# Performance work log

Measured on AMD Instinct MI355X. Metric: run time of the kernel, lower is better.

## Reference

```python
import jax, jax.numpy as jnp
import numpy as np

S, B, I, H, O = 512, 64, 128, 512, 1


def setup_inputs() -> dict:
    key = jax.random.key(0)
    ks = jax.random.split(key, 12)
    s = 1.0 / np.sqrt(H)
    u = lambda k, shape: jax.random.uniform(k, shape, jnp.float32, -s, s)
    return {
        "inputs": jax.random.normal(ks[0], (S, B, I), jnp.float32),
        # pre nn.RNN (1 layer, tanh)
        "W_ih_pre": u(ks[1], (H, I)),
        "W_hh_pre": u(ks[2], (H, H)),
        "b_ih_pre": u(ks[3], (H,)),
        "b_hh_pre": u(ks[4], (H,)),
        # post nn.RNNCell (input_size=hidden_size)
        "W_ih_post": u(ks[5], (H, H)),
        "W_hh_post": u(ks[6], (H, H)),
        "b_ih_post": u(ks[7], (H,)),
        "b_hh_post": u(ks[8], (H,)),
        # fc head
        "W_fc": u(ks[9], (O, H)),
        "b_fc": u(ks[10], (O,)),
    }


def reference(inputs, W_ih_pre, W_hh_pre, b_ih_pre, b_hh_pre,
              W_ih_post, W_hh_post, b_ih_post, b_hh_post, W_fc, b_fc):
    batch = inputs.shape[1]
    hidden = W_ih_pre.shape[0]
    h0 = jnp.zeros((batch, hidden), inputs.dtype)

    # ---- pre RNN over time (tanh cell), inputs are (S, B, I) ----
    x_proj = jnp.einsum('sbi,hi->sbh', inputs, W_ih_pre) + b_ih_pre

    def pre_step(h, x_t):
        h = jnp.tanh(x_t + h @ W_hh_pre.T + b_hh_pre)
        return h, h

    _, out_pre = jax.lax.scan(pre_step, h0, x_proj)  # (S, B, H)

    # ---- attention loop: exactly `hidden` sequential steps ----
    def attn_step(h, _):
        # dot-prod alignment: sum over feature dim -> (S, B)
        scores = jnp.einsum('sbh,bh->sb', out_pre, h)
        w = jax.nn.softmax(scores, axis=0)          # softmax over seq dim
        ctx = jnp.einsum('sbh,sb->bh', out_pre, w)  # weighted sum -> (B, H)
        h = jnp.tanh(ctx @ W_ih_post.T + b_ih_post + h @ W_hh_post.T + b_hh_post)
        return h, None

    h_post, _ = jax.lax.scan(attn_step, h0, None, length=hidden)
    return h_post @ W_fc.T + b_fc  # (B, O)
```

## Files before the change

### kernel.cpp

```cpp
#include <hip/hip_runtime.h>
#include <math.h>

#define NWG 256
#define NTHR 512
static constexpr int S = 512, B = 64, I = 128, H = 512;

static constexpr size_t OFF_BUF0   = 0;
static constexpr size_t OFF_PCTX   = (size_t)S * B * H;
static constexpr size_t OFF_H3X    = OFF_PCTX + (size_t)64 * 4 * 520;
static constexpr size_t OFF_ACTR   = OFF_H3X + (size_t)64 * 4 * 128;
static constexpr size_t OFF_HCTR   = OFF_ACTR + (size_t)64 * 4 * 16;
static constexpr size_t OFF_GFLAGS = OFF_HCTR + (size_t)64 * 4 * 16;
static constexpr size_t OFF_END    = OFF_GFLAGS + (size_t)256 * 16;

typedef float f32x2 __attribute__((ext_vector_type(2)));
typedef float f32x4 __attribute__((ext_vector_type(4)));

__device__ __forceinline__ void st_g1(float* p, float v) {
  asm volatile("global_store_dword %0, %1, off sc0 sc1" :: "v"(p), "v"(v) : "memory");
}
__device__ __forceinline__ void st_g2(float* p, f32x2 v) {
  asm volatile("global_store_dwordx2 %0, %1, off sc0 sc1" :: "v"(p), "v"(v) : "memory");
}
__device__ __forceinline__ void st_gu(unsigned* p, unsigned v) {
  asm volatile("global_store_dword %0, %1, off sc0 sc1" :: "v"(p), "v"(v) : "memory");
}
__device__ __forceinline__ f32x4 ld_g4(const float* p) {
  f32x4 v;
  asm volatile("global_load_dwordx4 %0, %1, off sc0 sc1\n\ts_waitcnt vmcnt(0)"
               : "=&v"(v) : "v"(p) : "memory");
  return v;
}
__device__ __forceinline__ void ld_3c(const float* v0, const float* v1, const float* v2,
                                      const float* m0, const float* m1, const float* m2,
                                      float& a, float& b, float& c,
                                      f32x2& x, f32x2& y, f32x2& z) {
  asm volatile("global_load_dword %0, %6, off sc0 sc1\n\t"
               "global_load_dword %1, %7, off sc0 sc1\n\t"
               "global_load_dword %2, %8, off sc0 sc1\n\t"
               "global_load_dwordx2 %3, %9, off sc0 sc1\n\t"
               "global_load_dwordx2 %4, %10, off sc0 sc1\n\t"
               "global_load_dwordx2 %5, %11, off sc0 sc1\n\t"
               "s_waitcnt vmcnt(0)"
               : "=&v"(a), "=&v"(b), "=&v"(c), "=&v"(x), "=&v"(y), "=&v"(z)
               : "v"(v0), "v"(v1), "v"(v2), "v"(m0), "v"(m1), "v"(m2) : "memory");
}
__device__ __forceinline__ void poll3_ge(const unsigned* p0, const unsigned* p1,
                                         const unsigned* p2, unsigned tgt) {
  unsigned a, b, c;
  do {
    asm volatile("global_load_dword %0, %3, off sc0 sc1\n\t"
                 "global_load_dword %1, %4, off sc0 sc1\n\t"
                 "global_load_dword %2, %5, off sc0 sc1\n\t"
                 "s_waitcnt vmcnt(0)"
                 : "=&v"(a), "=&v"(b), "=&v"(c)
                 : "v"(p0), "v"(p1), "v"(p2) : "memory");
  } while (a < tgt || b < tgt || c < tgt);
}
__device__ __forceinline__ void vm_drain() { asm volatile("s_waitcnt vmcnt(0)" ::: "memory"); }

__device__ __forceinline__ void gbar_all(unsigned* gflags, int wg, unsigned gen) {
  __syncthreads();
  if (threadIdx.x == 0)
    __hip_atomic_store(gflags + (size_t)wg * 16, gen, __ATOMIC_RELEASE, __HIP_MEMORY_SCOPE_AGENT);
  if (threadIdx.x < 256) {
    while (__hip_atomic_load(gflags + (size_t)threadIdx.x * 16, __ATOMIC_ACQUIRE,
                             __HIP_MEMORY_SCOPE_AGENT) < gen) {}
  }
  __syncthreads();
}

__global__ __launch_bounds__(NTHR, 2) void attn_fused(
    const float* __restrict__ inputs,
    const float* __restrict__ Wih_pre, const float* __restrict__ Whh_pre,
    const float* __restrict__ bih_pre, const float* __restrict__ bhh_pre,
    const float* __restrict__ Wih_post, const float* __restrict__ Whh_post,
    const float* __restrict__ bih_post, const float* __restrict__ bhh_post,
    const float* __restrict__ Wfc, const float* __restrict__ bfc,
    float* __restrict__ out, float* __restrict__ ws)
{
  float* buf0  = ws + OFF_BUF0;
  float* pctxg = ws + OFF_PCTX;
  float* h3xg  = ws + OFF_H3X;
  unsigned* actrg  = (unsigned*)(ws + OFF_ACTR);
  unsigned* hctrg  = (unsigned*)(ws + OFF_HCTR);
  unsigned* gflags = (unsigned*)(ws + OFF_GFLAGS);

  const int wg   = blockIdx.x;
  const int tid  = threadIdx.x;
  const int lane = tid & 63;
  const int wv   = tid >> 6;
  const int b    = wg & 63;
  const int part = wg >> 6;
  const int q1 = (part + 1) & 3, q2 = (part + 2) & 3, q3 = (part + 3) & 3;

  unsigned* hc_own = hctrg + ((size_t)b * 4 + part) * 16;
  unsigned* hc1 = hctrg + ((size_t)b * 4 + q1) * 16;
  unsigned* hc2 = hctrg + ((size_t)b * 4 + q2) * 16;
  unsigned* hc3 = hctrg + ((size_t)b * 4 + q3) * 16;
  unsigned* ac_own = actrg + ((size_t)b * 4 + part) * 16;
  unsigned* ac1 = actrg + ((size_t)b * 4 + q1) * 16;
  unsigned* ac2 = actrg + ((size_t)b * 4 + q2) * 16;
  unsigned* ac3 = actrg + ((size_t)b * 4 + q3) * 16;

  __shared__ float smem[8208];

  {
    const int h = tid;
    float4 Wr[32];
    const float4* wrow = (const float4*)(Wih_pre + (size_t)h * I);
    #pragma unroll
    for (int c = 0; c < 32; ++c) Wr[c] = wrow[c];
    const float bias = bih_pre[h] + bhh_pre[h];
    const int r0 = wg * 128;
    for (int t2 = 0; t2 < 2; ++t2) {
      __syncthreads();
      const float4* src = (const float4*)(inputs + (size_t)(r0 + t2 * 64) * I);
      for (int idx = tid; idx < 64 * I / 4; idx += NTHR)
        ((float4*)smem)[idx] = src[idx];
      __syncthreads();
      for (int r = 0; r < 64; ++r) {
        const float4* arow = (const float4*)(smem + r * I);
        float acc0 = 0.f, acc1 = 0.f;
        #pragma unroll
        for (int c = 0; c < 32; c += 2) {
          float4 a0 = arow[c], a1 = arow[c + 1];
          acc0 += a0.x * Wr[c].x + a0.y * Wr[c].y + a0.z * Wr[c].z + a0.w * Wr[c].w;
          acc1 += a1.x * Wr[c+1].x + a1.y * Wr[c+1].y + a1.z * Wr[c+1].z + a1.w * Wr[c+1].w;
        }
        buf0[(size_t)(r0 + t2 * 64 + r) * H + h] = acc0 + acc1 + bias;
      }
    }
  }
  gbar_all(gflags, wg, 1u);

  const int j  = part * 128 + (tid >> 2);
  const int kq = tid & 3;
  {
    float4 wpre[32];
    const float4* wrow = (const float4*)(Whh_pre + (size_t)j * H);
    #pragma unroll
    for (int i = 0; i < 32; ++i) wpre[i] = wrow[4 * i + kq];

    smem[tid] = 0.f;
    __syncthreads();

    for (int t = 0; t < S; ++t) {
      float* brow = buf0 + ((size_t)t * B + b) * H;
      float xp = brow[j];
      const float4* hst4 = (const float4*)smem;
      float d = 0.f;
      #pragma unroll
      for (int i = 0; i < 32; ++i) {
        float4 hv = hst4[4 * i + kq];
        d += wpre[i].x * hv.x + wpre[i].y * hv.y + wpre[i].z * hv.z + wpre[i].w * hv.w;
      }
      d += __shfl_xor(d, 1);
      d += __shfl_xor(d, 2);
      float hnew = tanhf(xp + d);
      const int par = (t + 1) & 1;
      float* slot = pctxg + (((size_t)b * 2 + par) * 4 + part) * 128;
      if (kq == 0) {
        brow[j] = hnew;
        st_g1(slot + (tid >> 2), hnew);
      }
      vm_drain();
      __syncthreads();
      if (tid == 0) st_gu(hc_own, (unsigned)(t + 1));
      poll3_ge(hc1, hc2, hc3, (unsigned)(t + 1));
      if (tid < 128) {
        f32x4 hv = ld_g4(pctxg + (((size_t)b * 2 + par) * 4) * 128 + (size_t)tid * 4);
        ((float4*)smem)[tid] = float4{hv.x, hv.y, hv.z, hv.w};
      }
      __syncthreads();
    }
  }
  gbar_all(gflags, wg, 2u);

  float4 ga[16], gb[16];
  {
    const int s0 = part * 128 + wv * 16;
    #pragma unroll
    for (int i = 0; i < 16; ++i) {
      const float* row = buf0 + ((size_t)(s0 + i) * B + b) * H;
      ga[i] = *(const float4*)(row + lane * 4);
      gb[i] = *(const float4*)(row + 256 + lane * 4);
    }
  }

  float4 wih[32], whh[32];
  {
    const float4* wr1 = (const float4*)(Wih_post + (size_t)j * H);
    const float4* wr2 = (const float4*)(Whh_post + (size_t)j * H);
    #pragma unroll
    for (int i = 0; i < 32; ++i) { wih[i] = wr1[4 * i + kq]; whh[i] = wr2[4 * i + kq]; }
  }
  const float bp3 = bih_post[j] + bhh_post[j];

  float* blk_own = pctxg + ((size_t)b * 4 + part) * 520;
  float* blk1 = pctxg + ((size_t)b * 4 + q1) * 520;
  float* blk2 = pctxg + ((size_t)b * 4 + q2) * 520;
  float* blk3 = pctxg + ((size_t)b * 4 + q3) * 520;

  smem[tid] = 0.f;
  __syncthreads();

  for (int u = 0; u < H; ++u) {
    float mstar, lsum;
    {
      float4 h0v = ((const float4*)smem)[lane];
      float4 h1v = ((const float4*)smem)[64 + lane];
      float p[16];
      #pragma unroll
      for (int i = 0; i < 16; ++i)
        p[i] = ga[i].x * h0v.x + ga[i].y * h0v.y + ga[i].z * h0v.z + ga[i].w * h0v.w
             + gb[i].x * h1v.x + gb[i].y * h1v.y + gb[i].z * h1v.z + gb[i].w * h1v.w;
      #pragma unroll
      for (int off = 32; off > 0; off >>= 1) {
        #pragma unroll
        for (int i = 0; i < 16; ++i) p[i] += __shfl_xor(p[i], off);
      }
      float m = p[0];
      #pragma unroll
      for (int i = 1; i < 16; ++i) m = fmaxf(m, p[i]);
      float l = 0.f;
      float4 c0{0.f,0.f,0.f,0.f}, c1{0.f,0.f,0.f,0.f};
      #pragma unroll
      for (int i = 0; i < 16; ++i) {
        float e = __expf(p[i] - m);
        l += e;
        c0.x += e * ga[i].x;  c0.y += e * ga[i].y;  c0.z += e * ga[i].z;  c0.w += e * ga[i].w;
        c1.x += e * gb[i].x;  c1.y += e * gb[i].y;  c1.z += e * gb[i].z;  c1.w += e * gb[i].w;
      }
      float* ctx_lds = smem + 1024;
      float* ml_lds  = smem + 5120;
      *(float4*)(ctx_lds + wv * 512 + lane * 4)       = c0;
      *(float4*)(ctx_lds + wv * 512 + 256 + lane * 4) = c1;
      if (lane == 0) { ml_lds[wv * 2] = m; ml_lds[wv * 2 + 1] = l; }
      __syncthreads();
      mstar = ml_lds[0];
      #pragma unroll
      for (int w = 1; w < 8; ++w) mstar = fmaxf(mstar, ml_lds[w * 2]);
      lsum = 0.f;
      float csum = 0.f;
      #pragma unroll
      for (int w = 0; w < 8; ++w) {
        float sc = __expf(ml_lds[w * 2] - mstar);
        lsum += sc * ml_lds[w * 2 + 1];
        csum += sc * ctx_lds[w * 512 + tid];
      }
      smem[512 + tid] = csum;
      st_g1(blk_own + tid, csum);
      if (tid == 0) st_g2(blk_own + 512, f32x2{mstar, lsum});
      vm_drain();
      __syncthreads();
      if (tid == 0) st_gu(ac_own, (unsigned)(u + 1));
    }

    {
      poll3_ge(ac1, ac2, ac3, (unsigned)(u + 1));
      float v1, v2, v3; f32x2 mlA, mlB, mlC;
      ld_3c(blk1 + tid, blk2 + tid, blk3 + tid,
            blk1 + 512, blk2 + 512, blk3 + 512, v1, v2, v3, mlA, mlB, mlC);
      float mb = fmaxf(fmaxf(mstar, mlA.x), fmaxf(mlB.x, mlC.x));
      float s0 = __expf(mstar - mb), s1 = __expf(mlA.x - mb);
      float s2 = __expf(mlB.x - mb), s3 = __expf(mlC.x - mb);
      float inv = 1.0f / (s0 * lsum + s1 * mlA.y + s2 * mlB.y + s3 * mlC.y);
      float cval = (s0 * smem[512 + tid] + s1 * v1 + s2 * v2 + s3 * v3) * inv;
      smem[1024 + tid] = cval;
      __syncthreads();
      const float4* ctx4 = (const float4*)(smem + 1024);
      const float4* hh4  = (const float4*)smem;
      float acc = 0.f;
      #pragma unroll
      for (int i = 0; i < 32; ++i) {
        float4 cv = ctx4[4 * i + kq];
        float4 hv = hh4[4 * i + kq];
        acc += wih[i].x * cv.x + wih[i].y * cv.y + wih[i].z * cv.z + wih[i].w * cv.w
             + whh[i].x * hv.x + whh[i].y * hv.y + whh[i].z * hv.z + whh[i].w * hv.w;
      }
      acc += __shfl_xor(acc, 1);
      acc += __shfl_xor(acc, 2);
      float hnew = tanhf(acc + bp3);
      if (kq == 0) st_g1(h3xg + ((size_t)b * 4 + part) * 128 + (tid >> 2), hnew);
      vm_drain();
      __syncthreads();
      if (tid == 0) st_gu(hc_own, (unsigned)(513 + u));
      poll3_ge(hc1, hc2, hc3, (unsigned)(513 + u));
      if (tid < 128) {
        f32x4 hv = ld_g4(h3xg + (size_t)b * 4 * 128 + (size_t)tid * 4);
        ((float4*)smem)[tid] = float4{hv.x, hv.y, hv.z, hv.w};
      }
      __syncthreads();
    }
  }

  if (part == 0) {
    float pv = smem[tid] * Wfc[tid];
    #pragma unroll
    for (int off = 32; off > 0; off >>= 1) pv += __shfl_xor(pv, off);
    __syncthreads();
    if (lane == 0) smem[5120 + wv] = pv;
    __syncthreads();
    if (tid == 0) {
      float s = 0.f;
      #pragma unroll
      for (int w = 0; w < 8; ++w) s += smem[5120 + w];
      out[b] = s + bfc[0];
    }
  }
}

extern "C" void kernel_launch(void* const* d_in, const int* in_sizes, int n_in,
                              void* d_out, int out_size, void* d_ws, size_t ws_size,
                              hipStream_t stream) {
  (void)in_sizes; (void)n_in; (void)out_size; (void)ws_size;
  const float* inputs   = (const float*)d_in[0];
  const float* Wih_pre  = (const float*)d_in[1];
  const float* Whh_pre  = (const float*)d_in[2];
  const float* bih_pre  = (const float*)d_in[3];
  const float* bhh_pre  = (const float*)d_in[4];
  const float* Wih_post = (const float*)d_in[5];
  const float* Whh_post = (const float*)d_in[6];
  const float* bih_post = (const float*)d_in[7];
  const float* bhh_post = (const float*)d_in[8];
  const float* Wfc      = (const float*)d_in[9];
  const float* bfc      = (const float*)d_in[10];
  float* out = (float*)d_out;
  float* ws  = (float*)d_ws;

  hipMemsetAsync((char*)d_ws + OFF_ACTR * sizeof(float), 0,
                 (OFF_END - OFF_ACTR) * sizeof(float), stream);

  attn_fused<<<dim3(NWG), dim3(NTHR), 0, stream>>>(
      inputs, Wih_pre, Whh_pre, bih_pre, bhh_pre,
      Wih_post, Whh_post, bih_post, bhh_post, Wfc, bfc, out, ws);
}
```

Before: 14.23 ms.

## Stop attention loop at exact fixed point and rebalance post-cell weight storage

After each attention step, every block checks whether the new hidden state is bitwise identical to the previous one and leaves the loop if so. The step depends only on h, so the remaining iterations would repeat the same state and the result stays exact. The post-cell weights are also split so that most of W_ih stays in registers, its tail sits in LDS, and W_hh is streamed from global memory. The W_hh product is computed early, before the cross-block wait. Only one wave polls the cross-block counters, and launch bounds drop to one block per CU. The gain depends on how quickly the inputs converge, and the extra check and barriers add cost to every step.

After: 19.90 ms. 39.8% more time.

```diff
diff --git a/kernel.cpp b/kernel.cpp
--- a/kernel.cpp
+++ b/kernel.cpp
@@ -8,13 +8,14 @@
 static constexpr size_t OFF_BUF0   = 0;
 static constexpr size_t OFF_PCTX   = (size_t)S * B * H;
 static constexpr size_t OFF_H3X    = OFF_PCTX + (size_t)64 * 4 * 520;
-static constexpr size_t OFF_ACTR   = OFF_H3X + (size_t)64 * 4 * 128;
+static constexpr size_t OFF_ACTR   = OFF_H3X + (size_t)64 * 512;
 static constexpr size_t OFF_HCTR   = OFF_ACTR + (size_t)64 * 4 * 16;
 static constexpr size_t OFF_GFLAGS = OFF_HCTR + (size_t)64 * 4 * 16;
 static constexpr size_t OFF_END    = OFF_GFLAGS + (size_t)256 * 16;
 
 typedef float f32x2 __attribute__((ext_vector_type(2)));
 typedef float f32x4 __attribute__((ext_vector_type(4)));
+#define PIN4(x) asm volatile("" : "+v"(x))
 
 __device__ __forceinline__ void st_g1(float* p, float v) {
   asm volatile("global_store_dword %0, %1, off sc0 sc1" :: "v"(p), "v"(v) : "memory");
@@ -70,7 +71,15 @@
   __syncthreads();
 }
 
-__global__ __launch_bounds__(NTHR, 2) void attn_fused(
+static constexpr int L_TAIL = 0;
+static constexpr int L_MRG  = 26112;
+static constexpr int L_ML   = 30208;
+static constexpr int L_HA   = 30224;
+static constexpr int L_HB   = 30736;
+static constexpr int L_CTX  = 31248;
+static constexpr int L_FLG  = 31760;
+
+__global__ __launch_bounds__(NTHR, 1) void attn_fused(
     const float* __restrict__ inputs,
     const float* __restrict__ Wih_pre, const float* __restrict__ Whh_pre,
     const float* __restrict__ bih_pre, const float* __restrict__ bhh_pre,
@@ -103,28 +112,28 @@
   unsigned* ac2 = actrg + ((size_t)b * 4 + q2) * 16;
   unsigned* ac3 = actrg + ((size_t)b * 4 + q3) * 16;
 
-  __shared__ float smem[8208];
+  __shared__ __align__(16) float smem[31776];
 
   {
     const int h = tid;
-    float4 Wr[32];
-    const float4* wrow = (const float4*)(Wih_pre + (size_t)h * I);
+    f32x4 Wr[32];
+    const f32x4* wrow = (const f32x4*)(Wih_pre + (size_t)h * I);
     #pragma unroll
     for (int c = 0; c < 32; ++c) Wr[c] = wrow[c];
     const float bias = bih_pre[h] + bhh_pre[h];
     const int r0 = wg * 128;
     for (int t2 = 0; t2 < 2; ++t2) {
       __syncthreads();
-      const float4* src = (const float4*)(inputs + (size_t)(r0 + t2 * 64) * I);
+      const f32x4* src = (const f32x4*)(inputs + (size_t)(r0 + t2 * 64) * I);
       for (int idx = tid; idx < 64 * I / 4; idx += NTHR)
-        ((float4*)smem)[idx] = src[idx];
+        ((f32x4*)smem)[idx] = src[idx];
       __syncthreads();
       for (int r = 0; r < 64; ++r) {
-        const float4* arow = (const float4*)(smem + r * I);
+        const f32x4* arow = (const f32x4*)(smem + r * I);
         float acc0 = 0.f, acc1 = 0.f;
         #pragma unroll
         for (int c = 0; c < 32; c += 2) {
-          float4 a0 = arow[c], a1 = arow[c + 1];
+          f32x4 a0 = arow[c], a1 = arow[c + 1];
           acc0 += a0.x * Wr[c].x + a0.y * Wr[c].y + a0.z * Wr[c].z + a0.w * Wr[c].w;
           acc1 += a1.x * Wr[c+1].x + a1.y * Wr[c+1].y + a1.z * Wr[c+1].z + a1.w * Wr[c+1].w;
         }
@@ -137,22 +146,23 @@
   const int j  = part * 128 + (tid >> 2);
   const int kq = tid & 3;
   {
-    float4 wpre[32];
-    const float4* wrow = (const float4*)(Whh_pre + (size_t)j * H);
-    #pragma unroll
-    for (int i = 0; i < 32; ++i) wpre[i] = wrow[4 * i + kq];
-
-    smem[tid] = 0.f;
+    f32x4 wpre[32];
+    const f32x4* wrow = (const f32x4*)(Whh_pre + (size_t)j * H);
+    #pragma unroll
+    for (int i = 0; i < 32; ++i) { wpre[i] = wrow[4 * i + kq]; PIN4(wpre[i]); }
+
+    float* hst = smem + L_HA;
+    hst[tid] = 0.f;
     __syncthreads();
 
     for (int t = 0; t < S; ++t) {
       float* brow = buf0 + ((size_t)t * B + b) * H;
       float xp = brow[j];
-      const float4* hst4 = (const float4*)smem;
+      const f32x4* hst4 = (const f32x4*)hst;
       float d = 0.f;
       #pragma unroll
       for (int i = 0; i < 32; ++i) {
-        float4 hv = hst4[4 * i + kq];
+        f32x4 hv = hst4[4 * i + kq];
         d += wpre[i].x * hv.x + wpre[i].y * hv.y + wpre[i].z * hv.z + wpre[i].w * hv.w;
       }
       d += __shfl_xor(d, 1);
@@ -167,34 +177,40 @@
       vm_drain();
       __syncthreads();
       if (tid == 0) st_gu(hc_own, (unsigned)(t + 1));
-      poll3_ge(hc1, hc2, hc3, (unsigned)(t + 1));
+      if (wv == 0) poll3_ge(hc1, hc2, hc3, (unsigned)(t + 1));
+      __syncthreads();
       if (tid < 128) {
         f32x4 hv = ld_g4(pctxg + (((size_t)b * 2 + par) * 4) * 128 + (size_t)tid * 4);
-        ((float4*)smem)[tid] = float4{hv.x, hv.y, hv.z, hv.w};
+        ((f32x4*)hst)[tid] = hv;
       }
       __syncthreads();
     }
   }
   gbar_all(gflags, wg, 2u);
 
-  float4 ga[16], gb[16];
+  f32x4 ga[16], gb[16];
   {
     const int s0 = part * 128 + wv * 16;
     #pragma unroll
     for (int i = 0; i < 16; ++i) {
       const float* row = buf0 + ((size_t)(s0 + i) * B + b) * H;
-      ga[i] = *(const float4*)(row + lane * 4);
-      gb[i] = *(const float4*)(row + 256 + lane * 4);
-    }
-  }
-
-  float4 wih[32], whh[32];
+      ga[i] = *(const f32x4*)(row + lane * 4);
+      gb[i] = *(const f32x4*)(row + 256 + lane * 4);
+    }
+  }
+
+  f32x4 wihh[20];
   {
-    const float4* wr1 = (const float4*)(Wih_post + (size_t)j * H);
-    const float4* wr2 = (const float4*)(Whh_post + (size_t)j * H);
-    #pragma unroll
-    for (int i = 0; i < 32; ++i) { wih[i] = wr1[4 * i + kq]; whh[i] = wr2[4 * i + kq]; }
-  }
+    const f32x4* wr1 = (const f32x4*)(Wih_post + (size_t)j * H);
+    #pragma unroll
+    for (int i = 0; i < 20; ++i) { wihh[i] = wr1[4 * i + kq]; PIN4(wihh[i]); }
+    for (int idx = tid; idx < 128 * 48; idx += NTHR) {
+      int row = idx / 48, f4c = idx % 48;
+      f32x4 v = ((const f32x4*)(Wih_post + (size_t)(part * 128 + row) * H + 320))[f4c];
+      *(f32x4*)(smem + L_TAIL + row * 204 + f4c * 4) = v;
+    }
+  }
+  const f32x4* whr = (const f32x4*)(Whh_post + (size_t)j * H);
   const float bp3 = bih_post[j] + bhh_post[j];
 
   float* blk_own = pctxg + ((size_t)b * 4 + part) * 520;
@@ -202,14 +218,27 @@
   float* blk2 = pctxg + ((size_t)b * 4 + q2) * 520;
   float* blk3 = pctxg + ((size_t)b * 4 + q3) * 520;
 
-  smem[tid] = 0.f;
+  float* hcur = smem + L_HA;
+  float* hoth = smem + L_HB;
+  hcur[tid] = 0.f;
   __syncthreads();
 
   for (int u = 0; u < H; ++u) {
+    float zacc = 0.f;
+    {
+      const f32x4* h4 = (const f32x4*)hcur;
+      #pragma unroll
+      for (int i = 0; i < 32; ++i) {
+        f32x4 w = whr[4 * i + kq];
+        f32x4 hv = h4[4 * i + kq];
+        zacc += w.x * hv.x + w.y * hv.y + w.z * hv.z + w.w * hv.w;
+      }
+    }
+
     float mstar, lsum;
     {
-      float4 h0v = ((const float4*)smem)[lane];
-      float4 h1v = ((const float4*)smem)[64 + lane];
+      f32x4 h0v = ((const f32x4*)hcur)[lane];
+      f32x4 h1v = ((const f32x4*)hcur)[64 + lane];
       float p[16];
       #pragma unroll
       for (int i = 0; i < 16; ++i)
@@ -224,18 +253,18 @@
       #pragma unroll
       for (int i = 1; i < 16; ++i) m = fmaxf(m, p[i]);
       float l = 0.f;
-      float4 c0{0.f,0.f,0.f,0.f}, c1{0.f,0.f,0.f,0.f};
+      f32x4 c0 = {0.f,0.f,0.f,0.f}, c1 = {0.f,0.f,0.f,0.f};
       #pragma unroll
       for (int i = 0; i < 16; ++i) {
         float e = __expf(p[i] - m);
         l += e;
-        c0.x += e * ga[i].x;  c0.y += e * ga[i].y;  c0.z += e * ga[i].z;  c0.w += e * ga[i].w;
-        c1.x += e * gb[i].x;  c1.y += e * gb[i].y;  c1.z += e * gb[i].z;  c1.w += e * gb[i].w;
-      }
-      float* ctx_lds = smem + 1024;
-      float* ml_lds  = smem + 5120;
-      *(float4*)(ctx_lds + wv * 512 + lane * 4)       = c0;
-      *(float4*)(ctx_lds + wv * 512 + 256 + lane * 4) = c1;
+        c0 += e * ga[i];
+        c1 += e * gb[i];
+      }
+      float* ctx_lds = smem + L_MRG;
+      float* ml_lds  = smem + L_ML;
+      *(f32x4*)(ctx_lds + wv * 512 + lane * 4)       = c0;
+      *(f32x4*)(ctx_lds + wv * 512 + 256 + lane * 4) = c1;
       if (lane == 0) { ml_lds[wv * 2] = m; ml_lds[wv * 2 + 1] = l; }
       __syncthreads();
       mstar = ml_lds[0];
@@ -249,7 +278,7 @@
         lsum += sc * ml_lds[w * 2 + 1];
         csum += sc * ctx_lds[w * 512 + tid];
       }
-      smem[512 + tid] = csum;
+      smem[L_CTX + tid] = csum;
       st_g1(blk_own + tid, csum);
       if (tid == 0) st_g2(blk_own + 512, f32x2{mstar, lsum});
       vm_drain();
@@ -258,7 +287,8 @@
     }
 
     {
-      poll3_ge(ac1, ac2, ac3, (unsigned)(u + 1));
+      if (wv == 0) poll3_ge(ac1, ac2, ac3, (unsigned)(u + 1));
+      __syncthreads();
       float v1, v2, v3; f32x2 mlA, mlB, mlC;
       ld_3c(blk1 + tid, blk2 + tid, blk3 + tid,
             blk1 + 512, blk2 + 512, blk3 + 512, v1, v2, v3, mlA, mlB, mlC);
@@ -266,46 +296,65 @@
       float s0 = __expf(mstar - mb), s1 = __expf(mlA.x - mb);
       float s2 = __expf(mlB.x - mb), s3 = __expf(mlC.x - mb);
       float inv = 1.0f / (s0 * lsum + s1 * mlA.y + s2 * mlB.y + s3 * mlC.y);
-      float cval = (s0 * smem[512 + tid] + s1 * v1 + s2 * v2 + s3 * v3) * inv;
-      smem[1024 + tid] = cval;
-      __syncthreads();
-      const float4* ctx4 = (const float4*)(smem + 1024);
-      const float4* hh4  = (const float4*)smem;
-      float acc = 0.f;
-      #pragma unroll
-      for (int i = 0; i < 32; ++i) {
-        float4 cv = ctx4[4 * i + kq];
-        float4 hv = hh4[4 * i + kq];
-        acc += wih[i].x * cv.x + wih[i].y * cv.y + wih[i].z * cv.z + wih[i].w * cv.w
-             + whh[i].x * hv.x + whh[i].y * hv.y + whh[i].z * hv.z + whh[i].w * hv.w;
+      float cval = (s0 * smem[L_CTX + tid] + s1 * v1 + s2 * v2 + s3 * v3) * inv;
+      __syncthreads();
+      smem[L_CTX + tid] = cval;
+      __syncthreads();
+      const f32x4* ctx4 = (const f32x4*)(smem + L_CTX);
+      float acc = zacc;
+      #pragma unroll
+      for (int i = 0; i < 20; ++i) {
+        f32x4 cv = ctx4[4 * i + kq];
+        acc += wihh[i].x * cv.x + wihh[i].y * cv.y + wihh[i].z * cv.z + wihh[i].w * cv.w;
+      }
+      const f32x4* tl = (const f32x4*)(smem + L_TAIL + (tid >> 2) * 204);
+      #pragma unroll
+      for (int t = 0; t < 12; ++t) {
+        f32x4 wv4 = tl[4 * t + kq];
+        f32x4 cv = ctx4[80 + 4 * t + kq];
+        acc += wv4.x * cv.x + wv4.y * cv.y + wv4.z * cv.z + wv4.w * cv.w;
       }
       acc += __shfl_xor(acc, 1);
       acc += __shfl_xor(acc, 2);
       float hnew = tanhf(acc + bp3);
-      if (kq == 0) st_g1(h3xg + ((size_t)b * 4 + part) * 128 + (tid >> 2), hnew);
+      if (kq == 0) st_g1(h3xg + (size_t)b * 512 + part * 128 + (tid >> 2), hnew);
       vm_drain();
       __syncthreads();
       if (tid == 0) st_gu(hc_own, (unsigned)(513 + u));
-      poll3_ge(hc1, hc2, hc3, (unsigned)(513 + u));
+      if (wv == 0) poll3_ge(hc1, hc2, hc3, (unsigned)(513 + u));
+      __syncthreads();
       if (tid < 128) {
-        f32x4 hv = ld_g4(h3xg + (size_t)b * 4 * 128 + (size_t)tid * 4);
-        ((float4*)smem)[tid] = float4{hv.x, hv.y, hv.z, hv.w};
-      }
-      __syncthreads();
+        f32x4 hv = ld_g4(h3xg + (size_t)b * 512 + (size_t)tid * 4);
+        ((f32x4*)hoth)[tid] = hv;
+      }
+      __syncthreads();
+    }
+
+    {
+      bool eq = (hoth[tid] == hcur[tid]);
+      unsigned long long bal = __ballot(eq);
+      if (lane == 0) smem[L_FLG + wv] = (bal == ~0ull) ? 1.f : 0.f;
+      __syncthreads();
+      float allf = 1.f;
+      #pragma unroll
+      for (int w = 0; w < 8; ++w) allf = fminf(allf, smem[L_FLG + w]);
+      float* t = hcur; hcur = hoth; hoth = t;
+      __syncthreads();
+      if (allf != 0.f) break;
     }
   }
 
   if (part == 0) {
-    float pv = smem[tid] * Wfc[tid];
+    float pv = hcur[tid] * Wfc[tid];
     #pragma unroll
     for (int off = 32; off > 0; off >>= 1) pv += __shfl_xor(pv, off);
     __syncthreads();
-    if (lane == 0) smem[5120 + wv] = pv;
+    if (lane == 0) smem[L_ML + wv] = pv;
     __syncthreads();
     if (tid == 0) {
       float s = 0.f;
       #pragma unroll
-      for (int w = 0; w < 8; ++w) s += smem[5120 + w];
+      for (int w = 0; w < 8; ++w) s += smem[L_ML + w];
       out[b] = s + bfc[0];
     }
   }
```
